# Performance work log

Hardware: AMD Instinct MI355X
Metric: run time of the kernel (lower is better)

The kernel has to match this reference:

```python
import jax, jax.numpy as jnp
import numpy as np

L, B, S, E, H, FF = 4, 1, 2048, 768, 12, 3072
DH = E // H
EPS = 1e-5

def setup_inputs() -> dict:
    key = jax.random.key(0)
    ks = jax.random.split(key, 10)
    w = lambda k, shape: jax.random.normal(k, shape, jnp.float32) * 0.02
    return {
        "inputs_embeds": jax.random.normal(ks[0], (B, S, E), jnp.float32),
        "wpe": w(ks[1], (S, E)),
        "ln1_g": jnp.ones((L, E), jnp.float32), "ln1_b": jnp.zeros((L, E), jnp.float32),
        "Wq": w(ks[2], (L, E, E)), "bq": jnp.zeros((L, E), jnp.float32),
        "Wk": w(ks[3], (L, E, E)), "bk": jnp.zeros((L, E), jnp.float32),
        "Wv": w(ks[4], (L, E, E)), "bv": jnp.zeros((L, E), jnp.float32),
        "Wo": w(ks[5], (L, E, E)), "bo": jnp.zeros((L, E), jnp.float32),
        "ln2_g": jnp.ones((L, E), jnp.float32), "ln2_b": jnp.zeros((L, E), jnp.float32),
        "W1": w(ks[6], (L, E, FF)), "b1": jnp.zeros((L, FF), jnp.float32),
        "W2": w(ks[7], (L, FF, E)), "b2": jnp.zeros((L, E), jnp.float32),
        "lnf_g": jnp.ones((E,), jnp.float32), "lnf_b": jnp.zeros((E,), jnp.float32),
    }

def _layernorm(x, g, b):
    mu = jnp.mean(x, axis=-1, keepdims=True)
    var = jnp.mean(jnp.square(x - mu), axis=-1, keepdims=True)
    return (x - mu) * jax.lax.rsqrt(var + EPS) * g + b

def _block(x, p):
    (g1, b1_, wq, bq, wk, bk, wv, bv, wo, bo, g2, b2_, w1, bb1, w2, bb2) = p
    h = _layernorm(x, g1, b1_)
    Bq, Sq, _ = x.shape
    q = (h @ wq + bq).reshape(Bq, Sq, H, DH)
    k = (h @ wk + bk).reshape(Bq, Sq, H, DH)
    v = (h @ wv + bv).reshape(Bq, Sq, H, DH)
    scale = DH ** (-0.5)
    # no softmax: purely linear scale * Q K^T V (attn_weights unused downstream)
    attn_w = jnp.einsum('bqhd,bkhd->bhqk', q, k) * scale  # [B,H,S,S]
    a = jnp.einsum('bhqk,bkhd->bqhd', attn_w, v).reshape(Bq, Sq, E)
    x = x + (a @ wo + bo)
    h2 = _layernorm(x, g2, b2_)
    mlp = jax.nn.gelu(h2 @ w1 + bb1, approximate=False) @ w2 + bb2
    return x + mlp

def reference(inputs_embeds, wpe, ln1_g, ln1_b, Wq, bq, Wk, bk, Wv, bv, Wo, bo,
              ln2_g, ln2_b, W1, b1, W2, b2, lnf_g, lnf_b):
    seq = inputs_embeds.shape[1]
    x = inputs_embeds + wpe[:seq]  # dropout p=0 -> identity
    layer_params = (ln1_g, ln1_b, Wq, bq, Wk, bk, Wv, bv, Wo, bo,
                    ln2_g, ln2_b, W1, b1, W2, b2)
    def body(carry, p):
        return _block(carry, p), None
    x, _ = jax.lax.scan(body, x, layer_params)
    return _layernorm(x, lnf_g, lnf_b)
```

## Files before the change

kernel.cpp:

```cpp
#include <hip/hip_runtime.h>
#include <hip/hip_bf16.h>
#include <math.h>

#define SS 2048
#define EE 768
#define HH 12
#define DHH 64
#define FFF 3072
#define LL 4

typedef __hip_bfloat16 bf16;
typedef __attribute__((ext_vector_type(8))) short short8;
typedef __attribute__((ext_vector_type(4))) float f32x4;

__device__ __forceinline__ float b2f(short u) {
  union { unsigned int i; float f; } v;
  v.i = ((unsigned int)(unsigned short)u) << 16;
  return v.f;
}
__device__ __forceinline__ bf16 f2b(float f) { return __float2bfloat16(f); }
__device__ __forceinline__ unsigned int f2bu(float f) {
  return (unsigned int)__bfloat16_as_ushort(__float2bfloat16(f));
}

__device__ __forceinline__ void async_ld16(const void* g, void* l) {
  __builtin_amdgcn_global_load_lds(
      (const __attribute__((address_space(1))) void*)g,
      (__attribute__((address_space(3))) void*)l, 16, 0, 0);
}

template <typename OutT>
__global__ __launch_bounds__(256) void ln_fused_kernel(
    float* x, const float* __restrict__ bias, const float* __restrict__ part,
    int nparts, const float* __restrict__ extra,
    const float* __restrict__ g, const float* __restrict__ bta,
    int writeback, int readx, OutT* __restrict__ out) {
  int row = blockIdx.x;
  int tid = threadIdx.x;
  float* xr = x + (size_t)row * EE;
  float v0 = 0.f, v1 = 0.f, v2 = 0.f;
  if (readx) { v0 = xr[tid]; v1 = xr[tid + 256]; v2 = xr[tid + 512]; }
  if (bias) { v0 += bias[tid]; v1 += bias[tid + 256]; v2 += bias[tid + 512]; }
  for (int p = 0; p < nparts; p++) {
    const float* pr = part + (size_t)p * SS * EE + (size_t)row * EE;
    v0 += pr[tid]; v1 += pr[tid + 256]; v2 += pr[tid + 512];
  }
  if (extra) {
    const float* er = extra + (size_t)row * EE;
    v0 += er[tid]; v1 += er[tid + 256]; v2 += er[tid + 512];
  }
  if (writeback) { xr[tid] = v0; xr[tid + 256] = v1; xr[tid + 512] = v2; }
  float s  = v0 + v1 + v2;
  float s2 = v0 * v0 + v1 * v1 + v2 * v2;
  #pragma unroll
  for (int off = 32; off >= 1; off >>= 1) {
    s  += __shfl_down(s,  off);
    s2 += __shfl_down(s2, off);
  }
  __shared__ float red[8];
  __shared__ float mb[2];
  int lane = tid & 63, wid = tid >> 6;
  if (lane == 0) { red[wid] = s; red[4 + wid] = s2; }
  __syncthreads();
  if (tid == 0) {
    float ts  = red[0] + red[1] + red[2] + red[3];
    float ts2 = red[4] + red[5] + red[6] + red[7];
    float mu  = ts * (1.0f / EE);
    float var = ts2 * (1.0f / EE) - mu * mu;
    mb[0] = mu; mb[1] = rsqrtf(var + 1e-5f);
  }
  __syncthreads();
  float mu = mb[0], rs = mb[1];
  OutT* orow = out + (size_t)row * EE;
  float o0 = (v0 - mu) * rs * g[tid]       + bta[tid];
  float o1 = (v1 - mu) * rs * g[tid + 256] + bta[tid + 256];
  float o2 = (v2 - mu) * rs * g[tid + 512] + bta[tid + 512];
  if constexpr (sizeof(OutT) == 4) {
    orow[tid] = o0; orow[tid + 256] = o1; orow[tid + 512] = o2;
  } else {
    orow[tid] = f2b(o0); orow[tid + 256] = f2b(o1); orow[tid + 512] = f2b(o2);
  }
}

__global__ __launch_bounds__(256) void transpose_all_kernel(
    const float* __restrict__ Wq, const float* __restrict__ Wk,
    const float* __restrict__ Wv, const float* __restrict__ Wo,
    const float* __restrict__ W1, const float* __restrict__ W2,
    bf16* __restrict__ WtAll) {
  __shared__ unsigned int lds[32][33];
  int bid = blockIdx.x;
  int l = bid / 3456, r = bid % 3456;
  bf16* base = WtAll + (size_t)l * 7077888;
  const float* src; bf16* dst; int K, N, rr;
  if (r < 864) {
    int m = r / 288; rr = r % 288;
    src = (m == 0 ? Wq : m == 1 ? Wk : Wv) + (size_t)l * EE * EE;
    dst = base + (size_t)m * 589824; K = 768; N = 768;
  } else if (r < 1152) {
    rr = r - 864; src = Wo + (size_t)l * EE * EE; dst = base + 1769472; K = 768; N = 768;
  } else if (r < 2304) {
    rr = r - 1152; src = W1 + (size_t)l * EE * FFF; dst = base + 2359296; K = 768; N = 3072;
  } else {
    rr = r - 2304; src = W2 + (size_t)l * FFF * EE; dst = base + 4718592; K = 3072; N = 768;
  }
  int ntn = N >> 5;
  int k0 = (rr / ntn) * 64, n0 = (rr % ntn) * 32;
  int kp = threadIdx.x >> 3, ns = (threadIdx.x & 7) * 4;
  const float* s0 = src + (size_t)(k0 + 2 * kp) * N + n0 + ns;
  float4 e = *(const float4*)s0;
  float4 o = *(const float4*)(s0 + N);
  lds[ns + 0][kp] = (f2bu(o.x) << 16) | f2bu(e.x);
  lds[ns + 1][kp] = (f2bu(o.y) << 16) | f2bu(e.y);
  lds[ns + 2][kp] = (f2bu(o.z) << 16) | f2bu(e.z);
  lds[ns + 3][kp] = (f2bu(o.w) << 16) | f2bu(e.w);
  __syncthreads();
  int n = threadIdx.x >> 3, kp4 = (threadIdx.x & 7) * 4;
  uint4 ov;
  ov.x = lds[n][kp4];     ov.y = lds[n][kp4 + 1];
  ov.z = lds[n][kp4 + 2]; ov.w = lds[n][kp4 + 3];
  unsigned int* d = (unsigned int*)dst + (size_t)(n0 + n) * (K >> 1) + (k0 >> 1) + kp4;
  *(uint4*)d = ov;
}

__global__ __launch_bounds__(256) void concat_bias_all_kernel(
    const float* __restrict__ bq, const float* __restrict__ bk,
    const float* __restrict__ bv, float* __restrict__ out) {
  int g = blockIdx.x * 256 + threadIdx.x;
  int l = g / 2304, i = g % 2304;
  out[g] = (i < 768) ? bq[l * 768 + i]
         : (i < 1536 ? bk[l * 768 + i - 768] : bv[l * 768 + i - 1536]);
}

__global__ __launch_bounds__(256) void gemm128_kernel(
    const bf16* __restrict__ A, int lda, const bf16* __restrict__ Bt,
    const float* __restrict__ bias, void* __restrict__ Cv, void* __restrict__ Cv2,
    float* __restrict__ part, int K, int N, int mode, int Ksplit) {
  __shared__ __align__(16) short As[128 * 64];
  __shared__ __align__(16) short Bs[128 * 64];
  const int t = threadIdx.x;
  const int wave = t >> 6, lane = t & 63;
  const int m0 = blockIdx.y * 128, n0 = blockIdx.x * 128;

  const int srow = t >> 3;
  const int sw   = (t & 7) ^ (srow & 7);
  const bf16* Ag = A  + (size_t)(m0 + srow) * lda + sw * 8;
  const bf16* Bg = Bt + (size_t)(n0 + srow) * K + sw * 8;

  const int fr = lane & 15, kq = lane >> 4;
  const int wm = (wave >> 1) * 64, wn = (wave & 1) * 64;
  f32x4 acc[4][4] = {};

  int kBeg = 0, kEnd = K;
  if (mode == 2) { kBeg = blockIdx.z * Ksplit; kEnd = kBeg + Ksplit; }

  for (int k0 = kBeg; k0 < kEnd; k0 += 64) {
    #pragma unroll
    for (int q = 0; q < 4; q++) {
      async_ld16(Ag + (size_t)(q * 32) * lda + k0, As + q * 2048 + wave * 512);
      async_ld16(Bg + (size_t)(q * 32) * K  + k0, Bs + q * 2048 + wave * 512);
    }
    __syncthreads();
    #pragma unroll
    for (int s = 0; s < 2; s++) {
      short8 a[4], b[4];
      #pragma unroll
      for (int i = 0; i < 4; i++) {
        int r = wm + 16 * i + fr;
        int p = (kq + 4 * s) ^ (r & 7);
        a[i] = *(const short8*)(As + r * 64 + p * 8);
      }
      #pragma unroll
      for (int j = 0; j < 4; j++) {
        int r = wn + 16 * j + fr;
        int p = (kq + 4 * s) ^ (r & 7);
        b[j] = *(const short8*)(Bs + r * 64 + p * 8);
      }
      #pragma unroll
      for (int i = 0; i < 4; i++)
        #pragma unroll
        for (int j = 0; j < 4; j++)
          acc[i][j] = __builtin_amdgcn_mfma_f32_16x16x32_bf16(a[i], b[j], acc[i][j], 0, 0, 0);
    }
    __syncthreads();
  }

  #pragma unroll
  for (int i = 0; i < 4; i++) {
    #pragma unroll
    for (int j = 0; j < 4; j++) {
      const int r0 = m0 + wm + 16 * i + kq * 4;
      const int c  = n0 + wn + 16 * j + fr;
      if (mode == 2) {
        #pragma unroll
        for (int ri = 0; ri < 4; ri++)
          part[(size_t)blockIdx.z * SS * EE + (size_t)(r0 + ri) * EE + c] =
              acc[i][j][ri];
      } else if (mode == 4) {
        const float bv = bias[c];
        if (n0 < 768) {
          #pragma unroll
          for (int ri = 0; ri < 4; ri++)
            ((bf16*)Cv)[(size_t)(r0 + ri) * 768 + c] = f2b(acc[i][j][ri] + bv);
        } else {
          __align__(8) bf16 tb[4];
          #pragma unroll
          for (int ri = 0; ri < 4; ri++) tb[ri] = f2b(acc[i][j][ri] + bv);
          *(short4*)((short*)Cv2 + ((size_t)(c - 768) << 11) + r0) = *(short4*)&tb[0];
        }
      } else {
        const float bv = bias[c];
        #pragma unroll
        for (int ri = 0; ri < 4; ri++) {
          float val = acc[i][j][ri] + bv;
          val = 0.5f * val * (1.0f + erff(val * 0.70710678118654752f));
          ((bf16*)Cv)[(size_t)(r0 + ri) * N + c] = f2b(val);
        }
      }
    }
  }
}

__global__ __launch_bounds__(256) void gemm_resid_kernel(
    const bf16* __restrict__ A, int lda, const bf16* __restrict__ Bt,
    const float* __restrict__ bias, float* __restrict__ x, int K) {
  __shared__ __align__(16) short As[64 * 64];
  __shared__ __align__(16) short Bs[64 * 64];
  const int t = threadIdx.x;
  const int wave = t >> 6, lane = t & 63;
  const int m0 = blockIdx.y * 64, n0 = blockIdx.x * 64;

  const int srow = t >> 3;
  const int sw   = (t & 7) ^ (srow & 7);
  const bf16* Ag = A  + (size_t)(m0 + srow) * lda + sw * 8;
  const bf16* Bg = Bt + (size_t)(n0 + srow) * K + sw * 8;

  const int fr = lane & 15, kq = lane >> 4;
  const int wm = (wave >> 1) * 32, wn = (wave & 1) * 32;
  f32x4 acc[2][2] = {};

  for (int k0 = 0; k0 < K; k0 += 64) {
    async_ld16(Ag + k0,                    As + wave * 512);
    async_ld16(Ag + (size_t)32 * lda + k0, As + 2048 + wave * 512);
    async_ld16(Bg + k0,                    Bs + wave * 512);
    async_ld16(Bg + (size_t)32 * K + k0,   Bs + 2048 + wave * 512);
    __syncthreads();
    #pragma unroll
    for (int s = 0; s < 2; s++) {
      short8 a[2], b[2];
      #pragma unroll
      for (int i = 0; i < 2; i++) {
        int r = wm + 16 * i + fr;
        int p = (kq + 4 * s) ^ (r & 7);
        a[i] = *(const short8*)(As + r * 64 + p * 8);
      }
      #pragma unroll
      for (int j = 0; j < 2; j++) {
        int r = wn + 16 * j + fr;
        int p = (kq + 4 * s) ^ (r & 7);
        b[j] = *(const short8*)(Bs + r * 64 + p * 8);
      }
      #pragma unroll
      for (int i = 0; i < 2; i++)
        #pragma unroll
        for (int j = 0; j < 2; j++)
          acc[i][j] = __builtin_amdgcn_mfma_f32_16x16x32_bf16(a[i], b[j], acc[i][j], 0, 0, 0);
    }
    __syncthreads();
  }

  #pragma unroll
  for (int i = 0; i < 2; i++) {
    #pragma unroll
    for (int j = 0; j < 2; j++) {
      const int r0 = m0 + wm + 16 * i + kq * 4;
      const int c  = n0 + wn + 16 * j + fr;
      const float bv = bias[c];
      #pragma unroll
      for (int ri = 0; ri < 4; ri++) {
        const size_t idx = (size_t)(r0 + ri) * EE + c;
        x[idx] = acc[i][j][ri] + bv + x[idx];
      }
    }
  }
}

__global__ __launch_bounds__(256) void attn_fused_kernel(
    const bf16* __restrict__ kvT, const bf16* __restrict__ Wo_t,
    bf16* __restrict__ Gt) {
  __shared__ short pbuf[4][4096];
  __shared__ short Ms[4096];
  const int nt = blockIdx.x, h = blockIdx.y;
  const int lane = threadIdx.x & 63, wave = threadIdx.x >> 6;
  const int fr = lane & 15, kq = lane >> 4;
  const short* kT = (const short*)kvT + (size_t)h * 64 * 2048;
  const short* vT = (const short*)kvT + (size_t)(768 + h * 64) * 2048;

  f32x4 acc[4][4] = {};
  for (int it = 0; it < 8; it++) {
    const int s0 = (it * 4 + wave) * 64;
    #pragma unroll
    for (int s = 0; s < 2; s++) {
      short8 a[4], b[4];
      #pragma unroll
      for (int i = 0; i < 4; i++)
        a[i] = *(const short8*)(kT + (size_t)(16 * i + fr) * 2048 + s0 + s * 32 + kq * 8);
      #pragma unroll
      for (int j = 0; j < 4; j++)
        b[j] = *(const short8*)(vT + (size_t)(16 * j + fr) * 2048 + s0 + s * 32 + kq * 8);
      #pragma unroll
      for (int i = 0; i < 4; i++)
        #pragma unroll
        for (int j = 0; j < 4; j++)
          acc[i][j] = __builtin_amdgcn_mfma_f32_16x16x32_bf16(a[i], b[j], acc[i][j], 0, 0, 0);
    }
  }
  #pragma unroll
  for (int i = 0; i < 4; i++)
    #pragma unroll
    for (int j = 0; j < 4; j++)
      #pragma unroll
      for (int ri = 0; ri < 4; ri++)
        pbuf[wave][(16 * i + kq * 4 + ri) * 64 + 16 * j + fr] =
            (short)__bfloat16_as_ushort(f2b(acc[i][j][ri]));
  __syncthreads();
  {
    int e0 = threadIdx.x * 16;
    #pragma unroll
    for (int e = 0; e < 16; e++) {
      float s = b2f(pbuf[0][e0 + e]) + b2f(pbuf[1][e0 + e]) +
                b2f(pbuf[2][e0 + e]) + b2f(pbuf[3][e0 + e]);
      Ms[e0 + e] = (short)__bfloat16_as_ushort(f2b(s * 0.125f));
    }
  }
  __syncthreads();

  const int nb = nt * 128 + wave * 32;
  f32x4 g[4][2] = {};
  #pragma unroll
  for (int s = 0; s < 2; s++) {
    short8 a[4], b[2];
    #pragma unroll
    for (int i = 0; i < 4; i++)
      a[i] = *(const short8*)(Ms + (16 * i + fr) * 64 + s * 32 + kq * 8);
    #pragma unroll
    for (int j = 0; j < 2; j++)
      b[j] = *(const short8*)((const short*)Wo_t +
             (size_t)(nb + 16 * j + fr) * 768 + h * 64 + s * 32 + kq * 8);
    #pragma unroll
    for (int i = 0; i < 4; i++)
      #pragma unroll
      for (int j = 0; j < 2; j++)
        g[i][j] = __builtin_amdgcn_mfma_f32_16x16x32_bf16(a[i], b[j], g[i][j], 0, 0, 0);
  }
  #pragma unroll
  for (int i = 0; i < 4; i++)
    #pragma unroll
    for (int j = 0; j < 2; j++) {
      const int c = nb + 16 * j + fr;
      const int d1 = 16 * i + kq * 4;
      __align__(8) bf16 tb[4];
      #pragma unroll
      for (int ri = 0; ri < 4; ri++) tb[ri] = f2b(g[i][j][ri]);
      *(short4*)((short*)Gt + (size_t)c * 768 + h * 64 + d1) = *(short4*)&tb[0];
    }
}

extern "C" void kernel_launch(void* const* d_in, const int* in_sizes, int n_in,
                              void* d_out, int out_size, void* d_ws, size_t ws_size,
                              hipStream_t stream) {
  const float* emb  = (const float*)d_in[0];
  const float* wpe  = (const float*)d_in[1];
  const float* ln1g = (const float*)d_in[2];
  const float* ln1b = (const float*)d_in[3];
  const float* Wq   = (const float*)d_in[4];
  const float* bq   = (const float*)d_in[5];
  const float* Wk   = (const float*)d_in[6];
  const float* bk   = (const float*)d_in[7];
  const float* Wv   = (const float*)d_in[8];
  const float* bv   = (const float*)d_in[9];
  const float* Wo   = (const float*)d_in[10];
  const float* bo   = (const float*)d_in[11];
  const float* ln2g = (const float*)d_in[12];
  const float* ln2b = (const float*)d_in[13];
  const float* W1   = (const float*)d_in[14];
  const float* b1   = (const float*)d_in[15];
  const float* W2   = (const float*)d_in[16];
  const float* b2   = (const float*)d_in[17];
  const float* lnfg = (const float*)d_in[18];
  const float* lnfb = (const float*)d_in[19];

  char* w = (char*)d_ws;
  bf16*  WtAll = (bf16*)w;   w += (size_t)4 * 7077888 * 2;
  float* bqkvA = (float*)w;  w += (size_t)4 * 2304 * 4;
  float* x     = (float*)w;  w += (size_t)SS * EE * 4;
  bf16*  hb    = (bf16*)w;   w += (size_t)SS * EE * 2;
  bf16*  qkvQ  = (bf16*)w;   w += (size_t)SS * EE * 2;
  bf16*  kvT   = (bf16*)w;   w += (size_t)1536 * 2048 * 2;
  bf16*  Gt    = (bf16*)w;   w += (size_t)EE * EE * 2;
  bf16*  mb2   = (bf16*)w;   w += (size_t)SS * FFF * 2;
  float* cpart = (float*)w;  w += (size_t)4 * SS * EE * 4;

  dim3 blk(256);
  transpose_all_kernel<<<13824, blk, 0, stream>>>(Wq, Wk, Wv, Wo, W1, W2, WtAll);
  concat_bias_all_kernel<<<36, blk, 0, stream>>>(bq, bk, bv, bqkvA);

  for (int l = 0; l < LL; l++) {
    bf16* Wl = WtAll + (size_t)l * 7077888;
    bf16* Wqkv_t = Wl;
    bf16* Wo_t   = Wl + 1769472;
    bf16* W1_t   = Wl + 2359296;
    bf16* W2_t   = Wl + 4718592;

    if (l == 0) {
      ln_fused_kernel<bf16><<<SS, blk, 0, stream>>>(
          x, nullptr, emb, 1, wpe, ln1g, ln1b, 1, 0, hb);
    } else {
      ln_fused_kernel<bf16><<<SS, blk, 0, stream>>>(
          x, b2 + (l - 1) * EE, cpart, 4, nullptr,
          ln1g + l * EE, ln1b + l * EE, 1, 1, hb);
    }
    gemm128_kernel<<<dim3(18, 16), blk, 0, stream>>>(
        hb, EE, Wqkv_t, bqkvA + l * 2304, qkvQ, kvT, nullptr, EE, 2304, 4, 0);
    attn_fused_kernel<<<dim3(6, HH), blk, 0, stream>>>(kvT, Wo_t, Gt);
    gemm_resid_kernel<<<dim3(12, 32), blk, 0, stream>>>(
        qkvQ, EE, Gt, bo + l * EE, x, EE);
    ln_fused_kernel<bf16><<<SS, blk, 0, stream>>>(
        x, nullptr, nullptr, 0, nullptr, ln2g + l * EE, ln2b + l * EE, 0, 1, hb);
    gemm128_kernel<<<dim3(24, 16), blk, 0, stream>>>(
        hb, EE, W1_t, b1 + l * FFF, mb2, nullptr, nullptr, EE, FFF, 1, 0);
    gemm128_kernel<<<dim3(6, 16, 4), blk, 0, stream>>>(
        mb2, FFF, W2_t, nullptr, nullptr, nullptr, cpart, FFF, EE, 2, 768);
  }
  ln_fused_kernel<float><<<SS, blk, 0, stream>>>(
      x, b2 + 3 * EE, cpart, 4, nullptr, lnfg, lnfb, 0, 1, (float*)d_out);
}
```

Measured before the change: 656.3 us.

## Shrink GEMM M-tile to 64, split attention KV reduction across sequence chunks

The shared GEMM kernel moves from 128x128 to 64x128 tiles, doubling the block count for the QKV, W1 and W2 GEMMs. The W2 split-K goes from 4 to 3 chunks, and the downstream layernorm reads 3 partials. The fused attention kernel is split in two: one kernel computes K^T V over 4 sequence chunks per head into fp32 partials, and a second sums them and applies Wo. The goal is more parallelism on a GPU with many CUs, at the cost of less reuse per tile, an extra launch and an fp32 partial round-trip.

```diff
diff --git a/kernel.cpp b/kernel.cpp
--- a/kernel.cpp
+++ b/kernel.cpp
@@ -131,15 +131,15 @@
          : (i < 1536 ? bk[l * 768 + i - 768] : bv[l * 768 + i - 1536]);
 }
 
-__global__ __launch_bounds__(256) void gemm128_kernel(
+__global__ __launch_bounds__(256) void gemm_mn_kernel(
     const bf16* __restrict__ A, int lda, const bf16* __restrict__ Bt,
     const float* __restrict__ bias, void* __restrict__ Cv, void* __restrict__ Cv2,
     float* __restrict__ part, int K, int N, int mode, int Ksplit) {
-  __shared__ __align__(16) short As[128 * 64];
+  __shared__ __align__(16) short As[64 * 64];
   __shared__ __align__(16) short Bs[128 * 64];
   const int t = threadIdx.x;
   const int wave = t >> 6, lane = t & 63;
-  const int m0 = blockIdx.y * 128, n0 = blockIdx.x * 128;
+  const int m0 = blockIdx.y * 64, n0 = blockIdx.x * 128;
 
   const int srow = t >> 3;
   const int sw   = (t & 7) ^ (srow & 7);
@@ -147,24 +147,25 @@
   const bf16* Bg = Bt + (size_t)(n0 + srow) * K + sw * 8;
 
   const int fr = lane & 15, kq = lane >> 4;
-  const int wm = (wave >> 1) * 64, wn = (wave & 1) * 64;
-  f32x4 acc[4][4] = {};
+  const int wm = (wave >> 1) * 32, wn = (wave & 1) * 64;
+  f32x4 acc[2][4] = {};
 
   int kBeg = 0, kEnd = K;
   if (mode == 2) { kBeg = blockIdx.z * Ksplit; kEnd = kBeg + Ksplit; }
 
   for (int k0 = kBeg; k0 < kEnd; k0 += 64) {
-    #pragma unroll
-    for (int q = 0; q < 4; q++) {
-      async_ld16(Ag + (size_t)(q * 32) * lda + k0, As + q * 2048 + wave * 512);
-      async_ld16(Bg + (size_t)(q * 32) * K  + k0, Bs + q * 2048 + wave * 512);
-    }
+    async_ld16(Ag + k0,                    As + wave * 512);
+    async_ld16(Ag + (size_t)32 * lda + k0, As + 2048 + wave * 512);
+    async_ld16(Bg + k0,                    Bs + wave * 512);
+    async_ld16(Bg + (size_t)32 * K + k0,   Bs + 2048 + wave * 512);
+    async_ld16(Bg + (size_t)64 * K + k0,   Bs + 4096 + wave * 512);
+    async_ld16(Bg + (size_t)96 * K + k0,   Bs + 6144 + wave * 512);
     __syncthreads();
     #pragma unroll
     for (int s = 0; s < 2; s++) {
-      short8 a[4], b[4];
-      #pragma unroll
-      for (int i = 0; i < 4; i++) {
+      short8 a[2], b[4];
+      #pragma unroll
+      for (int i = 0; i < 2; i++) {
         int r = wm + 16 * i + fr;
         int p = (kq + 4 * s) ^ (r & 7);
         a[i] = *(const short8*)(As + r * 64 + p * 8);
@@ -176,7 +177,7 @@
         b[j] = *(const short8*)(Bs + r * 64 + p * 8);
       }
       #pragma unroll
-      for (int i = 0; i < 4; i++)
+      for (int i = 0; i < 2; i++)
         #pragma unroll
         for (int j = 0; j < 4; j++)
           acc[i][j] = __builtin_amdgcn_mfma_f32_16x16x32_bf16(a[i], b[j], acc[i][j], 0, 0, 0);
@@ -185,7 +186,7 @@
   }
 
   #pragma unroll
-  for (int i = 0; i < 4; i++) {
+  for (int i = 0; i < 2; i++) {
     #pragma unroll
     for (int j = 0; j < 4; j++) {
       const int r0 = m0 + wm + 16 * i + kq * 4;
@@ -284,20 +285,18 @@
   }
 }
 
-__global__ __launch_bounds__(256) void attn_fused_kernel(
-    const bf16* __restrict__ kvT, const bf16* __restrict__ Wo_t,
-    bf16* __restrict__ Gt) {
+__global__ __launch_bounds__(256) void attn_kv_kernel(
+    const bf16* __restrict__ kvT, float* __restrict__ Mpart) {
   __shared__ short pbuf[4][4096];
-  __shared__ short Ms[4096];
-  const int nt = blockIdx.x, h = blockIdx.y;
+  const int h = blockIdx.x, c = blockIdx.y;
   const int lane = threadIdx.x & 63, wave = threadIdx.x >> 6;
   const int fr = lane & 15, kq = lane >> 4;
   const short* kT = (const short*)kvT + (size_t)h * 64 * 2048;
   const short* vT = (const short*)kvT + (size_t)(768 + h * 64) * 2048;
 
   f32x4 acc[4][4] = {};
-  for (int it = 0; it < 8; it++) {
-    const int s0 = (it * 4 + wave) * 64;
+  for (int it = 0; it < 2; it++) {
+    const int s0 = c * 512 + (it * 4 + wave) * 64;
     #pragma unroll
     for (int s = 0; s < 2; s++) {
       short8 a[4], b[4];
@@ -325,12 +324,40 @@
   __syncthreads();
   {
     int e0 = threadIdx.x * 16;
+    float* Mp = Mpart + (((size_t)c * HH + h) << 12) + e0;
     #pragma unroll
     for (int e = 0; e < 16; e++) {
-      float s = b2f(pbuf[0][e0 + e]) + b2f(pbuf[1][e0 + e]) +
-                b2f(pbuf[2][e0 + e]) + b2f(pbuf[3][e0 + e]);
-      Ms[e0 + e] = (short)__bfloat16_as_ushort(f2b(s * 0.125f));
-    }
+      Mp[e] = b2f(pbuf[0][e0 + e]) + b2f(pbuf[1][e0 + e]) +
+              b2f(pbuf[2][e0 + e]) + b2f(pbuf[3][e0 + e]);
+    }
+  }
+}
+
+__global__ __launch_bounds__(256) void attn_wo_kernel(
+    const float* __restrict__ Mpart, const bf16* __restrict__ Wo_t,
+    bf16* __restrict__ Gt) {
+  __shared__ short Ms[4096];
+  const int nt = blockIdx.x, h = blockIdx.y;
+  const int lane = threadIdx.x & 63, wave = threadIdx.x >> 6;
+  const int fr = lane & 15, kq = lane >> 4;
+
+  {
+    int e0 = threadIdx.x * 16;
+    float s[16];
+    #pragma unroll
+    for (int e = 0; e < 16; e++) s[e] = 0.f;
+    #pragma unroll
+    for (int c = 0; c < 4; c++) {
+      const float* P = Mpart + (((size_t)c * HH + h) << 12) + e0;
+      #pragma unroll
+      for (int e = 0; e < 16; e += 4) {
+        float4 q = *(const float4*)(P + e);
+        s[e] += q.x; s[e + 1] += q.y; s[e + 2] += q.z; s[e + 3] += q.w;
+      }
+    }
+    #pragma unroll
+    for (int e = 0; e < 16; e++)
+      Ms[e0 + e] = (short)__bfloat16_as_ushort(f2b(s[e] * 0.125f));
   }
   __syncthreads();
 
@@ -398,7 +425,8 @@
   bf16*  kvT   = (bf16*)w;   w += (size_t)1536 * 2048 * 2;
   bf16*  Gt    = (bf16*)w;   w += (size_t)EE * EE * 2;
   bf16*  mb2   = (bf16*)w;   w += (size_t)SS * FFF * 2;
-  float* cpart = (float*)w;  w += (size_t)4 * SS * EE * 4;
+  float* cpart = (float*)w;  w += (size_t)3 * SS * EE * 4;
+  float* Mpart = (float*)w;  w += (size_t)4 * HH * 64 * 64 * 4;
 
   dim3 blk(256);
   transpose_all_kernel<<<13824, blk, 0, stream>>>(Wq, Wk, Wv, Wo, W1, W2, WtAll);
@@ -416,21 +444,22 @@
           x, nullptr, emb, 1, wpe, ln1g, ln1b, 1, 0, hb);
     } else {
       ln_fused_kernel<bf16><<<SS, blk, 0, stream>>>(
-          x, b2 + (l - 1) * EE, cpart, 4, nullptr,
+          x, b2 + (l - 1) * EE, cpart, 3, nullptr,
           ln1g + l * EE, ln1b + l * EE, 1, 1, hb);
     }
-    gemm128_kernel<<<dim3(18, 16), blk, 0, stream>>>(
+    gemm_mn_kernel<<<dim3(18, 32), blk, 0, stream>>>(
         hb, EE, Wqkv_t, bqkvA + l * 2304, qkvQ, kvT, nullptr, EE, 2304, 4, 0);
-    attn_fused_kernel<<<dim3(6, HH), blk, 0, stream>>>(kvT, Wo_t, Gt);
+    attn_kv_kernel<<<dim3(HH, 4), blk, 0, stream>>>(kvT, Mpart);
+    attn_wo_kernel<<<dim3(6, HH), blk, 0, stream>>>(Mpart, Wo_t, Gt);
     gemm_resid_kernel<<<dim3(12, 32), blk, 0, stream>>>(
         qkvQ, EE, Gt, bo + l * EE, x, EE);
     ln_fused_kernel<bf16><<<SS, blk, 0, stream>>>(
         x, nullptr, nullptr, 0, nullptr, ln2g + l * EE, ln2b + l * EE, 0, 1, hb);
-    gemm128_kernel<<<dim3(24, 16), blk, 0, stream>>>(
+    gemm_mn_kernel<<<dim3(24, 32), blk, 0, stream>>>(
         hb, EE, W1_t, b1 + l * FFF, mb2, nullptr, nullptr, EE, FFF, 1, 0);
-    gemm128_kernel<<<dim3(6, 16, 4), blk, 0, stream>>>(
-        mb2, FFF, W2_t, nullptr, nullptr, nullptr, cpart, FFF, EE, 2, 768);
+    gemm_mn_kernel<<<dim3(6, 32, 3), blk, 0, stream>>>(
+        mb2, FFF, W2_t, nullptr, nullptr, nullptr, cpart, FFF, EE, 2, 1024);
   }
   ln_fused_kernel<float><<<SS, blk, 0, stream>>>(
-      x, b2 + 3 * EE, cpart, 4, nullptr, lnfg, lnfb, 0, 1, (float*)d_out);
-}
+      x, b2 + 3 * EE, cpart, 3, nullptr, lnfg, lnfb, 0, 1, (float*)d_out);
+}
```

Measured after the change: 565.1 us. 1.16x faster.
